# Kernel tuning notes

Hardware: AMD Instinct MI355X
Metric: run time of the kernel (lower is better)

The kernel has to match this reference:

```python
import jax, jax.numpy as jnp
import numpy as np

B, P, D, N, H = 1, 256, 512, 8, 64
STD = 0.02
IGNORE = -1000000.0


def setup_inputs() -> dict:
    key = jax.random.key(0)
    ks = jax.random.split(key, 9)
    inp = {"normalized_resid_pre": jax.random.normal(ks[0], (B, P, D), jnp.float32)}
    for i, s in enumerate("ABCDE"):
        inp["W_" + s] = STD * jax.random.normal(ks[i + 1], (N, D, H), jnp.float32)
        inp["b_" + s] = jnp.zeros((N, H), jnp.float32)
    inp["W_V"] = STD * jax.random.normal(ks[6], (N, H, H, H), jnp.float32)
    inp["W_K"] = STD * jax.random.normal(ks[7], (N, H, H, H), jnp.float32)
    inp["W_O"] = STD * jax.random.normal(ks[8], (N, H, D), jnp.float32)
    inp["b_O"] = jnp.zeros((D,), jnp.float32)
    return inp


def reference(normalized_resid_pre, W_A, b_A, W_B, b_B, W_C, b_C, W_D, b_D, W_E, b_E, W_V, W_K, W_O, b_O):
    x = normalized_resid_pre
    b_sz = x.shape[0]
    proj = lambda W, b: jnp.einsum('ndh,bpd->bpnh', W, x) + b
    ta = proj(W_A, b_A)
    tb = proj(W_B, b_B)
    tc = proj(W_C, b_C)
    td = proj(W_D, b_D)
    te = proj(W_E, b_E)
    # V_Layer: v[b, p1, p2, n, h3]
    v = jnp.einsum('bpnh,bqng,nhgf->bpqnf', td, te, W_V)
    # TrittentionCScore: chained einsums -> scores[b, n, p, q, r]
    step1 = jnp.einsum('brnk,nijk->brij', tc, W_K)
    step2 = jnp.einsum('brij,bqnj->briq', step1, tb)
    scores = jnp.einsum('briq,bpni->bnpqr', step2, ta)
    # CausalMask (attn_eq=False, order_attn=True): mask over (t=p, s=q, q=r) dims
    ti = jnp.arange(P)[:, None, None]
    si = jnp.arange(P)[None, :, None]
    qi = jnp.arange(P)[None, None, :]
    mask = (ti >= qi) | (si >= qi) | (ti >= si)  # [P, P, P]
    scores = jnp.where(mask, IGNORE, scores)
    # TrittentionCPattern: b n p q r -> b n r (p q), /d_head, extra column, softmax
    flat = jnp.transpose(scores, (0, 1, 4, 2, 3)).reshape(b_sz, N, P, P * P) / H
    extra = jnp.full((b_sz, N, P, 1), -1000.0, flat.dtype)
    attn = jax.nn.softmax(jnp.concatenate([flat, extra], axis=-1), axis=-1)
    # Z_Layer: v -> b n h (p s), extra zero column, combine
    vf = jnp.transpose(v, (0, 3, 4, 1, 2)).reshape(b_sz, N, H, P * P)
    vf = jnp.concatenate([vf, jnp.zeros((b_sz, N, H, 1), vf.dtype)], axis=-1)
    z = jnp.einsum('bnql,bnhl->bqnh', attn, vf)
    # Result + Out
    zint = jnp.einsum('bqnh,nhd->bqnd', z, W_O)
    return zint.sum(axis=2) + b_O
```

## Files before the change

### kernel.cpp

```cpp
#include <hip/hip_runtime.h>
#include <hip/hip_bf16.h>


typedef __hip_bfloat16 bf16;
typedef __attribute__((ext_vector_type(8))) short short8;
typedef __attribute__((ext_vector_type(4))) short s16x4;
typedef __attribute__((ext_vector_type(4))) float floatx4;

__device__ __forceinline__ float ldf(const float* p){ return *p; }
__device__ __forceinline__ float ldf(const bf16* p){ return __bfloat162float(*p); }
__device__ __forceinline__ void  stf(float* p, float v){ *p = v; }
__device__ __forceinline__ void  stf(bf16*  p, float v){ *p = __float2bfloat16(v); }

__device__ __forceinline__ floatx4 mfma16(short8 a, short8 b, floatx4 c){
  return __builtin_amdgcn_mfma_f32_16x16x32_bf16(a, b, c, 0, 0, 0);
}
__device__ __forceinline__ short8 ld_g8(const bf16* p){
  return *reinterpret_cast<const short8*>(p);
}
__device__ __forceinline__ short bfs(float x){
  bf16 v = __float2bfloat16(x);
  return *reinterpret_cast<short*>(&v);
}

__device__ __forceinline__ bool is_bf16_x(const void* xv)
{
  const unsigned* x32 = (const unsigned*)xv;
  unsigned w = x32[threadIdx.x & 63];
  unsigned lo = w & 0xFFFFu;
  unsigned e  = (lo >> 7) & 0xFFu;
  bool v = (lo == 0u) || (e >= 90u && e <= 145u);
  unsigned long long m = __ballot(v);
  return __popcll(m) >= 40;
}

template<typename TI>
__device__ __forceinline__ void proj_body(
    const TI* __restrict__ x, const TI* const* Ws, const TI* const* bs,
    bf16* __restrict__ tproj, float* As, float* Bs)
{
  const int bz = blockIdx.z, j = bz >> 3, n = bz & 7;
  const TI* B    = Ws[j] + (size_t)n * 32768;
  const TI* bias = bs[j] + n * 64;
  bf16* out = tproj + (size_t)j * 131072;
  const int m0 = blockIdx.y * 64;
  const int t = threadIdx.x, tx = t & 15, ty = t >> 4;
  float acc[4][4] = {};
  for (int k0 = 0; k0 < 512; k0 += 16) {
    { int m = t >> 2, kk = (t & 3) * 4;
      const TI* ap = x + (size_t)(m0 + m) * 512 + (k0 + kk);
      float a0 = ldf(ap+0), a1 = ldf(ap+1), a2 = ldf(ap+2), a3 = ldf(ap+3);
      As[(kk+0)*68+m] = a0; As[(kk+1)*68+m] = a1;
      As[(kk+2)*68+m] = a2; As[(kk+3)*68+m] = a3; }
    { int kk = t >> 4, nn = (t & 15) * 4;
      const TI* bp = B + (size_t)(k0 + kk) * 64 + nn;
      Bs[kk*68+nn+0] = ldf(bp+0); Bs[kk*68+nn+1] = ldf(bp+1);
      Bs[kk*68+nn+2] = ldf(bp+2); Bs[kk*68+nn+3] = ldf(bp+3); }
    __syncthreads();
    #pragma unroll
    for (int kk = 0; kk < 16; kk++) {
      float4 a4 = *reinterpret_cast<const float4*>(&As[kk*68 + ty*4]);
      float4 b4 = *reinterpret_cast<const float4*>(&Bs[kk*68 + tx*4]);
      float av[4] = {a4.x,a4.y,a4.z,a4.w}, bv[4] = {b4.x,b4.y,b4.z,b4.w};
      #pragma unroll
      for (int im = 0; im < 4; im++)
        #pragma unroll
        for (int in = 0; in < 4; in++) acc[im][in] += av[im] * bv[in];
    }
    __syncthreads();
  }
  #pragma unroll
  for (int im = 0; im < 4; im++)
    #pragma unroll
    for (int in = 0; in < 4; in++) {
      float v = acc[im][in] + ldf(bias + tx*4 + in);
      int p = m0 + ty*4 + im, h = tx*4 + in;
      if (j < 3) out[(size_t)p * 512 + n*64 + h] = __float2bfloat16(v);
      else       out[(size_t)n * 16384 + (size_t)h * 256 + p] = __float2bfloat16(v);
    }
}

__global__ __launch_bounds__(256) void proj_all(
    const void* __restrict__ x,
    const void* W0, const void* b0, const void* W1, const void* b1,
    const void* W2, const void* b2, const void* W3, const void* b3,
    const void* W4, const void* b4, bf16* __restrict__ tproj)
{
  __shared__ float As[16*68];
  __shared__ float Bs[16*68];
  if (is_bf16_x(x)) {
    const bf16* Ws[5] = {(const bf16*)W0,(const bf16*)W1,(const bf16*)W2,
                         (const bf16*)W3,(const bf16*)W4};
    const bf16* bs[5] = {(const bf16*)b0,(const bf16*)b1,(const bf16*)b2,
                         (const bf16*)b3,(const bf16*)b4};
    proj_body<bf16>((const bf16*)x, Ws, bs, tproj, As, Bs);
  } else {
    const float* Ws[5] = {(const float*)W0,(const float*)W1,(const float*)W2,
                          (const float*)W3,(const float*)W4};
    const float* bs[5] = {(const float*)b0,(const float*)b1,(const float*)b2,
                          (const float*)b3,(const float*)b4};
    proj_body<float>((const float*)x, Ws, bs, tproj, As, Bs);
  }
}

template<typename TW>
__device__ __forceinline__ void s1t_body(
    const bf16* __restrict__ tc, const TW* __restrict__ WK,
    bf16* __restrict__ s1t)
{
  const int i = blockIdx.x;
  const int t = threadIdx.x, wid = t >> 6, lane = t & 63, quad = lane >> 4, l16 = lane & 15;
  const int rw = blockIdx.y * 64 + wid * 16;
  floatx4 acc[4];
  #pragma unroll
  for (int jt = 0; jt < 4; jt++) acc[jt] = (floatx4){0.f, 0.f, 0.f, 0.f};
  for (int kc = 0; kc < 16; kc++) {
    short8 af = ld_g8(tc + (size_t)(rw + l16) * 512 + kc*32 + quad*8);
    const int n = kc >> 1, kk = (kc & 1) * 32 + quad * 8;
    #pragma unroll
    for (int jt = 0; jt < 4; jt++) {
      const TW* bp = WK + ((size_t)(n*64 + i) * 64 + jt*16 + l16) * 64 + kk;
      short8 bf;
      if constexpr (sizeof(TW) == 2) {
        bf = ld_g8((const bf16*)bp);
      } else {
        float4 x0 = *reinterpret_cast<const float4*>(bp);
        float4 x1 = *reinterpret_cast<const float4*>(bp + 4);
        bf[0]=bfs(x0.x); bf[1]=bfs(x0.y); bf[2]=bfs(x0.z); bf[3]=bfs(x0.w);
        bf[4]=bfs(x1.x); bf[5]=bfs(x1.y); bf[6]=bfs(x1.z); bf[7]=bfs(x1.w);
      }
      acc[jt] = mfma16(af, bf, acc[jt]);
    }
  }
  #pragma unroll
  for (int jt = 0; jt < 4; jt++)
    #pragma unroll
    for (int reg = 0; reg < 4; reg++)
      s1t[(size_t)(rw + quad*4 + reg) * 4096 + i*64 + jt*16 + l16] =
          __float2bfloat16(acc[jt][reg]);
}

__global__ __launch_bounds__(256) void s1t_all(
    const void* __restrict__ x, const bf16* __restrict__ tb,
    const bf16* __restrict__ tc, const void* __restrict__ WK,
    bf16* __restrict__ tbsbf, bf16* __restrict__ s1t)
{
  if (blockIdx.y == 4) {
    int t = blockIdx.x * 256 + threadIdx.x;
    int q = t >> 6, j = t & 63;
    float s = 0.f;
    #pragma unroll
    for (int n = 0; n < 8; n++) s += ldf(tb + q*512 + n*64 + j);
    tbsbf[t] = __float2bfloat16(s * 0.015625f);
    return;
  }
  if (is_bf16_x(x)) s1t_body<bf16>(tc, (const bf16*)WK, s1t);
  else              s1t_body<float>(tc, (const float*)WK, s1t);
}

__global__ __launch_bounds__(256) void tri_attn(
    const bf16* __restrict__ ta,
    const bf16* __restrict__ tbsbf,
    const bf16* __restrict__ s1t,
    const bf16* __restrict__ tdT,
    const bf16* __restrict__ teT,
    bf16* __restrict__ Sbuf)
{
  __shared__ __align__(16) char smb[39936];
  const int bx = blockIdx.x;
  const int n = bx & 7;
  const int r = 255 - (bx >> 3);
  const int t = threadIdx.x;
  const int wid = t >> 6, lane = t & 63, quad = lane >> 4, l16 = lane & 15;
  bf16* srow = Sbuf + (size_t)n * 1048576 + (size_t)r * 4096;
  if (r < 2) {
    short8 zz = (short8){0,0,0,0,0,0,0,0};
    reinterpret_cast<short8*>(srow)[t]       = zz;
    reinterpret_cast<short8*>(srow)[t + 256] = zz;
    return;
  }
  const int nch  = ((r - 1) >> 5) + 1;
  const int rcap = nch * 32;

  {
    const bf16* s1r = s1t + (size_t)r * 4096;
    short8 bfr[4][2];
    #pragma unroll
    for (int it = 0; it < 4; it++)
      #pragma unroll
      for (int kc = 0; kc < 2; kc++)
        bfr[it][kc] = ld_g8(s1r + (it*16 + l16)*64 + kc*32 + quad*8);
    #pragma unroll
    for (int qt = 0; qt < 4; qt++) {
      const int q0 = wid * 64 + qt * 16;
      if (q0 >= rcap) continue;
      if (q0 >= r) {
        #pragma unroll
        for (int it = 0; it < 4; it++)
          #pragma unroll
          for (int reg = 0; reg < 4; reg++) {
            int q = q0 + quad*4 + reg;
            *reinterpret_cast<bf16*>(smb + q*136 + (it*16 + l16)*2) =
                __float2bfloat16(0.f);
          }
        continue;
      }
      short8 af0 = ld_g8(tbsbf + (q0 + l16)*64 + quad*8);
      short8 af1 = ld_g8(tbsbf + (q0 + l16)*64 + 32 + quad*8);
      #pragma unroll
      for (int it = 0; it < 4; it++) {
        floatx4 acc = {0.f, 0.f, 0.f, 0.f};
        acc = mfma16(af0, bfr[it][0], acc);
        acc = mfma16(af1, bfr[it][1], acc);
        #pragma unroll
        for (int reg = 0; reg < 4; reg++) {
          int q = q0 + quad*4 + reg;
          float v = (q >= 1 && q < r) ? acc[reg] : 0.f;
          *reinterpret_cast<bf16*>(smb + q*136 + (it*16 + l16)*2) = __float2bfloat16(v);
        }
      }
    }
  }
  short8 taf[4][2];
  #pragma unroll
  for (int pt = 0; pt < 4; pt++)
    #pragma unroll
    for (int kc = 0; kc < 2; kc++)
      taf[pt][kc] = ld_g8(ta + (size_t)((pt*4 + wid)*16 + l16)*512 + n*64
                             + kc*32 + quad*8);
  __syncthreads();

  floatx4 Tacc[4][4];
  #pragma unroll
  for (int pt = 0; pt < 4; pt++)
    #pragma unroll
    for (int gt = 0; gt < 4; gt++) Tacc[pt][gt] = (floatx4){0.f, 0.f, 0.f, 0.f};
  float Zp = 0.f;
  char* EwB = smb + 34816 + wid * 1152;
  for (int ch = 0; ch < nch; ch++) {
    const int qc = ch * 32;
    if (qc + 31 <= wid * 16) continue;
    short8 cfr[2][2];
    #pragma unroll
    for (int qt2 = 0; qt2 < 2; qt2++)
      #pragma unroll
      for (int kc = 0; kc < 2; kc++)
        cfr[qt2][kc] = *reinterpret_cast<const short8*>(
            smb + (qc + qt2*16 + l16)*136 + (kc*32 + quad*8)*2);
    short8 tef[4];
    #pragma unroll
    for (int gt = 0; gt < 4; gt++)
      tef[gt] = ld_g8(teT + (size_t)n*16384 + (gt*16 + l16)*256 + qc + quad*8);
    #pragma unroll
    for (int pt = 0; pt < 4; pt++) {
      const int ptb = (pt*4 + wid) * 16;
      if (ptb >= qc + 31) continue;
      #pragma unroll
      for (int qt2 = 0; qt2 < 2; qt2++) {
        const int qh = qc + qt2*16;
        char* erow0 = EwB + (quad*4)*72 + (qt2*16 + l16)*2;
        if (qh + 15 <= ptb) {
          #pragma unroll
          for (int reg = 0; reg < 4; reg++)
            *reinterpret_cast<bf16*>(erow0 + reg*72) = __float2bfloat16(0.f);
        } else {
          floatx4 acc = {0.f, 0.f, 0.f, 0.f};
          acc = mfma16(taf[pt][0], cfr[qt2][0], acc);
          acc = mfma16(taf[pt][1], cfr[qt2][1], acc);
          if (qh >= ptb + 16 && qh + 15 < r) {
            #pragma unroll
            for (int reg = 0; reg < 4; reg++) {
              float e = __expf(acc[reg]);
              Zp += e;
              *reinterpret_cast<bf16*>(erow0 + reg*72) = __float2bfloat16(e);
            }
          } else {
            #pragma unroll
            for (int reg = 0; reg < 4; reg++) {
              int p = ptb + quad*4 + reg;
              int q = qh + l16;
              float e = (p < q && q < r) ? __expf(acc[reg]) : 0.f;
              Zp += e;
              *reinterpret_cast<bf16*>(erow0 + reg*72) = __float2bfloat16(e);
            }
          }
        }
      }
      short8 ef = *reinterpret_cast<const short8*>(EwB + l16*72 + quad*16);
      __builtin_amdgcn_s_setprio(1);
      #pragma unroll
      for (int gt = 0; gt < 4; gt++)
        Tacc[pt][gt] = mfma16(ef, tef[gt], Tacc[pt][gt]);
      __builtin_amdgcn_s_setprio(0);
    }
  }
  #pragma unroll
  for (int off = 32; off; off >>= 1) Zp += __shfl_down(Zp, off);
  float* scr = reinterpret_cast<float*>(smb + 39424);
  if (lane == 0) scr[wid] = Zp;
  __syncthreads();
  const float rinv = 1.f / (scr[0] + scr[1] + scr[2] + scr[3]);

  #pragma unroll
  for (int pt = 0; pt < 4; pt++) {
    if ((pt*4 + wid)*16 >= rcap) continue;
    #pragma unroll
    for (int gt = 0; gt < 4; gt++)
      #pragma unroll
      for (int reg = 0; reg < 4; reg++) {
        int g = gt*16 + l16;
        int p = (pt*4 + wid)*16 + quad*4 + reg;
        *reinterpret_cast<bf16*>(smb + g*528 + p*2) = __float2bfloat16(Tacc[pt][gt][reg]);
      }
  }
  __syncthreads();

  {
    short8 Taf[8];
    #pragma unroll
    for (int kc = 0; kc < 8; kc++)
      if (kc < nch)
        Taf[kc] = *reinterpret_cast<const short8*>(
            smb + (wid*16 + l16)*528 + (kc*32 + quad*8)*2);
    #pragma unroll
    for (int ht = 0; ht < 4; ht++) {
      floatx4 acc = {0.f, 0.f, 0.f, 0.f};
      __builtin_amdgcn_s_setprio(1);
      #pragma unroll
      for (int kc = 0; kc < 8; kc++) {
        if (kc < nch) {
          short8 bfragd = ld_g8(tdT + (size_t)n*16384 + (ht*16 + l16)*256 + kc*32 + quad*8);
          acc = mfma16(Taf[kc], bfragd, acc);
        }
      }
      __builtin_amdgcn_s_setprio(0);
      #pragma unroll
      for (int reg = 0; reg < 4; reg++) {
        int g = wid*16 + quad*4 + reg, h = ht*16 + l16;
        srow[h*64 + g] = __float2bfloat16(acc[reg] * rinv);
      }
    }
  }
}

template<typename TW>
__device__ __forceinline__ void z_body(
    const bf16* __restrict__ Sbuf, const TW* __restrict__ WV,
    float* __restrict__ zpart, int kslice, char* lds)
{
  const int rt = blockIdx.x, n = blockIdx.y, ks = blockIdx.z;
  const int t = threadIdx.x, wid = t >> 6, lane = t & 63, quad = lane >> 4, l16 = lane & 15;
  const int rw = rt * 64 + wid * 16;
  const int k0 = ks * kslice;
  const TW*  wvn = WV   + (size_t)n * 262144;
  const bf16* sn = Sbuf + (size_t)n * 1048576;
  floatx4 acc[4];
  #pragma unroll
  for (int ft = 0; ft < 4; ft++) acc[ft] = (floatx4){0.f, 0.f, 0.f, 0.f};
  const int row = t >> 3, f8 = (t & 7) * 8;
  for (int kb = k0; kb < k0 + kslice; kb += 32) {
    { const TW* src = wvn + (size_t)(kb + row) * 64 + f8;
      short sv[8];
      if constexpr (sizeof(TW) == 2) {
        short8 v = ld_g8((const bf16*)src);
        #pragma unroll
        for (int j = 0; j < 8; j++) sv[j] = v[j];
      } else {
        float4 a = *reinterpret_cast<const float4*>(src);
        float4 b = *reinterpret_cast<const float4*>(src + 4);
        sv[0]=bfs(a.x); sv[1]=bfs(a.y); sv[2]=bfs(a.z); sv[3]=bfs(a.w);
        sv[4]=bfs(b.x); sv[5]=bfs(b.y); sv[6]=bfs(b.z); sv[7]=bfs(b.w);
      }
      short* dst = reinterpret_cast<short*>(lds + row*136 + f8*2);
      s16x4 lo = {sv[0],sv[1],sv[2],sv[3]}, hi = {sv[4],sv[5],sv[6],sv[7]};
      *reinterpret_cast<s16x4*>(dst)     = lo;
      *reinterpret_cast<s16x4*>(dst + 4) = hi;
    }
    __syncthreads();
    short8 af = ld_g8(sn + (size_t)(rw + l16) * 4096 + kb + quad*8);
    #pragma unroll
    for (int ft = 0; ft < 4; ft++) {
      short8 bfv;
      #pragma unroll
      for (int j = 0; j < 8; j++)
        bfv[j] = *reinterpret_cast<const short*>(
            lds + (quad*8 + j)*136 + (ft*16 + l16)*2);
      acc[ft] = mfma16(af, bfv, acc[ft]);
    }
    __syncthreads();
  }
  float* zp = zpart + (size_t)ks * 131072;
  #pragma unroll
  for (int ft = 0; ft < 4; ft++)
    #pragma unroll
    for (int reg = 0; reg < 4; reg++)
      zp[(size_t)(rw + quad*4 + reg) * 512 + n*64 + ft*16 + l16] = acc[ft][reg];
}

__global__ __launch_bounds__(256) void z_all(
    const void* __restrict__ x, const bf16* __restrict__ Sbuf,
    const void* __restrict__ WV, float* __restrict__ zpart, int kslice)
{
  __shared__ __align__(16) char lds[32 * 136];
  if (is_bf16_x(x)) z_body<bf16>(Sbuf, (const bf16*)WV, zpart, kslice, lds);
  else              z_body<float>(Sbuf, (const float*)WV, zpart, kslice, lds);
}

__global__ __launch_bounds__(256) void zred_kern(
    const float* __restrict__ zpart, bf16* __restrict__ zbb, int ks)
{
  int idx = blockIdx.x * 256 + threadIdx.x;
  float s = 0.f;
  for (int k = 0; k < ks; k++) s += zpart[(size_t)k * 131072 + idx];
  zbb[idx] = __float2bfloat16(s);
}

template<typename TB, typename TC>
__device__ __forceinline__ void gemm_body(
    const bf16* __restrict__ A, const TB* __restrict__ B, TC* __restrict__ C,
    const TB* __restrict__ bias, float* As, float* Bs)
{
  const int m0 = blockIdx.y * 64, n0 = blockIdx.x * 64;
  const int t = threadIdx.x, tx = t & 15, ty = t >> 4;
  float acc[4][4] = {};
  for (int k0 = 0; k0 < 512; k0 += 16) {
    { int m = t >> 2, kk = (t & 3) * 4;
      const bf16* ap = A + (size_t)(m0 + m) * 512 + (k0 + kk);
      float a0 = ldf(ap+0), a1 = ldf(ap+1), a2 = ldf(ap+2), a3 = ldf(ap+3);
      As[(kk+0)*68+m] = a0; As[(kk+1)*68+m] = a1;
      As[(kk+2)*68+m] = a2; As[(kk+3)*68+m] = a3; }
    { int kk = t >> 4, nn = (t & 15) * 4;
      const TB* bp = B + (size_t)(k0 + kk) * 512 + (n0 + nn);
      Bs[kk*68+nn+0] = ldf(bp+0); Bs[kk*68+nn+1] = ldf(bp+1);
      Bs[kk*68+nn+2] = ldf(bp+2); Bs[kk*68+nn+3] = ldf(bp+3); }
    __syncthreads();
    #pragma unroll
    for (int kk = 0; kk < 16; kk++) {
      float4 a4 = *reinterpret_cast<const float4*>(&As[kk*68 + ty*4]);
      float4 b4 = *reinterpret_cast<const float4*>(&Bs[kk*68 + tx*4]);
      float av[4] = {a4.x,a4.y,a4.z,a4.w}, bv[4] = {b4.x,b4.y,b4.z,b4.w};
      #pragma unroll
      for (int im = 0; im < 4; im++)
        #pragma unroll
        for (int in = 0; in < 4; in++) acc[im][in] += av[im] * bv[in];
    }
    __syncthreads();
  }
  #pragma unroll
  for (int im = 0; im < 4; im++) {
    TC* cp = C + (size_t)(m0 + ty*4 + im) * 512 + n0 + tx*4;
    #pragma unroll
    for (int in = 0; in < 4; in++) {
      float v = acc[im][in] + ldf(bias + n0 + tx*4 + in);
      stf(cp + in, v);
    }
  }
}

__global__ __launch_bounds__(256) void gemm_all(
    const void* __restrict__ x, const bf16* __restrict__ zbb,
    const void* __restrict__ WO, const void* __restrict__ bO,
    void* __restrict__ out)
{
  __shared__ float As[16*68];
  __shared__ float Bs[16*68];
  if (is_bf16_x(x))
    gemm_body<bf16, bf16>(zbb, (const bf16*)WO, (bf16*)out, (const bf16*)bO, As, Bs);
  else
    gemm_body<float, float>(zbb, (const float*)WO, (float*)out, (const float*)bO, As, Bs);
}

extern "C" void kernel_launch(void* const* d_in, const int* in_sizes, int n_in,
                              void* d_out, int out_size, void* d_ws, size_t ws_size,
                              hipStream_t stream)
{
  (void)in_sizes; (void)n_in; (void)out_size;
  char* wsb = (char*)d_ws;
  bf16* tproj = (bf16*)(wsb + 256);
  bf16* tbsbf = (bf16*)(wsb + 1310976);
  bf16* s1t   = (bf16*)(wsb + 1343744);
  bf16* zbb   = (bf16*)(wsb + 3440896);
  bf16* Sbuf  = (bf16*)(wsb + 4194304);
  const long TE = 131072;
  const bool bigws = (ws_size == 0) || (ws_size >= 25165824);
  const int  ks     = bigws ? 8 : 2;
  const int  kslice = 4096 / ks;
  float* zpart = (float*)(bigws ? (wsb + 20971520) : (wsb + 1343744));

  proj_all<<<dim3(1,4,40), 256, 0, stream>>>(
      d_in[0], d_in[1], d_in[2], d_in[3], d_in[4], d_in[5], d_in[6],
      d_in[7], d_in[8], d_in[9], d_in[10], tproj);
  s1t_all<<<dim3(64,5), 256, 0, stream>>>(
      d_in[0], tproj + 1*TE, tproj + 2*TE, d_in[12], tbsbf, s1t);
  tri_attn<<<2048, 256, 0, stream>>>(
      tproj, tbsbf, s1t, tproj + 3*TE, tproj + 4*TE, Sbuf);
  z_all<<<dim3(4,8,ks), 256, 0, stream>>>(
      d_in[0], Sbuf, d_in[11], zpart, kslice);
  zred_kern<<<512, 256, 0, stream>>>(zpart, zbb, ks);
  gemm_all<<<dim3(8,4), 256, 0, stream>>>(
      d_in[0], zbb, d_in[13], d_in[14], d_out);
}
```

Before: 255.8 us.

## Pre-transpose W_V, add direct-MFMA z kernel, fuse split-K reduce into output GEMM

W_V is transposed to bf16 in an extra branch of the s1t kernel, so a new zmm kernel can compute z with direct global MFMA loads and two K-slices instead of the LDS-staged eight-slice path. The zred pass is dropped by having the output GEMM sum the two fp32 partials while loading A. In tri_attn, the softmax-exp tiles now go through two LDS buffers so two p-tiles' exp phases come before their MFMA updates, which should improve instruction overlap. This costs extra LDS per block and a W_V transpose on every call, and the old path stays as a fallback for small workspaces.

```diff
diff --git a/kernel.cpp b/kernel.cpp
--- a/kernel.cpp
+++ b/kernel.cpp
@@ -143,20 +143,82 @@
 __global__ __launch_bounds__(256) void s1t_all(
     const void* __restrict__ x, const bf16* __restrict__ tb,
     const bf16* __restrict__ tc, const void* __restrict__ WK,
-    bf16* __restrict__ tbsbf, bf16* __restrict__ s1t)
-{
+    bf16* __restrict__ tbsbf, bf16* __restrict__ s1t,
+    const void* __restrict__ WV, bf16* __restrict__ WVT)
+{
+  __shared__ short tile[64][72];
+  const int t = threadIdx.x;
   if (blockIdx.y == 4) {
-    int t = blockIdx.x * 256 + threadIdx.x;
-    int q = t >> 6, j = t & 63;
+    int tt = blockIdx.x * 256 + t;
+    int q = tt >> 6, j = tt & 63;
     float s = 0.f;
     #pragma unroll
     for (int n = 0; n < 8; n++) s += ldf(tb + q*512 + n*64 + j);
-    tbsbf[t] = __float2bfloat16(s * 0.015625f);
+    tbsbf[tt] = __float2bfloat16(s * 0.015625f);
+    return;
+  }
+  if (blockIdx.y == 5) {
+    const int n = blockIdx.x >> 3, kg = blockIdx.x & 7;
+    const bool bfp = is_bf16_x(x);
+    for (int sub = 0; sub < 8; sub++) {
+      const int k0 = kg*512 + sub*64;
+      { int kr = t >> 2, f16 = (t & 3) * 16;
+        if (bfp) {
+          const bf16* src = (const bf16*)WV + ((size_t)n*4096 + k0 + kr)*64 + f16;
+          *reinterpret_cast<short8*>(&tile[kr][f16])   = ld_g8(src);
+          *reinterpret_cast<short8*>(&tile[kr][f16+8]) = ld_g8(src + 8);
+        } else {
+          const float* src = (const float*)WV + ((size_t)n*4096 + k0 + kr)*64 + f16;
+          #pragma unroll
+          for (int j = 0; j < 16; j++) tile[kr][f16+j] = bfs(src[j]);
+        } }
+      __syncthreads();
+      { int f = t >> 2, k16 = (t & 3) * 16;
+        short8 w0, w1;
+        #pragma unroll
+        for (int j = 0; j < 8; j++) { w0[j] = tile[k16+j][f]; w1[j] = tile[k16+8+j][f]; }
+        bf16* dst = WVT + ((size_t)n*64 + f)*4096 + k0 + k16;
+        *reinterpret_cast<short8*>(dst)     = w0;
+        *reinterpret_cast<short8*>(dst + 8) = w1; }
+      __syncthreads();
+    }
     return;
   }
   if (is_bf16_x(x)) s1t_body<bf16>(tc, (const bf16*)WK, s1t);
   else              s1t_body<float>(tc, (const float*)WK, s1t);
 }
+
+#define E_PHASE(PT, BUF)                                                      \
+  {                                                                           \
+    const int ptb_ = ((PT)*4 + wid) * 16;                                     \
+    for (int qt2 = 0; qt2 < 2; qt2++) {                                       \
+      const int qh = qc + qt2*16;                                             \
+      char* erow0 = (BUF) + (quad*4)*72 + (qt2*16 + l16)*2;                   \
+      if (qh + 15 <= ptb_) {                                                  \
+        for (int reg = 0; reg < 4; reg++)                                     \
+          *reinterpret_cast<bf16*>(erow0 + reg*72) = __float2bfloat16(0.f);   \
+      } else {                                                                \
+        floatx4 acc = {0.f, 0.f, 0.f, 0.f};                                   \
+        acc = mfma16(taf[PT][0], cfr[qt2][0], acc);                           \
+        acc = mfma16(taf[PT][1], cfr[qt2][1], acc);                           \
+        if (qh >= ptb_ + 16 && qh + 15 < r) {                                 \
+          for (int reg = 0; reg < 4; reg++) {                                 \
+            float e = __expf(acc[reg]);                                       \
+            Zp += e;                                                          \
+            *reinterpret_cast<bf16*>(erow0 + reg*72) = __float2bfloat16(e);   \
+          }                                                                   \
+        } else {                                                              \
+          for (int reg = 0; reg < 4; reg++) {                                 \
+            int p = ptb_ + quad*4 + reg;                                      \
+            int q = qh + l16;                                                 \
+            float e = (p < q && q < r) ? __expf(acc[reg]) : 0.f;              \
+            Zp += e;                                                          \
+            *reinterpret_cast<bf16*>(erow0 + reg*72) = __float2bfloat16(e);   \
+          }                                                                   \
+        }                                                                     \
+      }                                                                       \
+    }                                                                         \
+  }
 
 __global__ __launch_bounds__(256) void tri_attn(
     const bf16* __restrict__ ta,
@@ -166,7 +228,7 @@
     const bf16* __restrict__ teT,
     bf16* __restrict__ Sbuf)
 {
-  __shared__ __align__(16) char smb[39936];
+  __shared__ __align__(16) char smb[44544];
   const int bx = blockIdx.x;
   const int n = bx & 7;
   const int r = 255 - (bx >> 3);
@@ -236,7 +298,8 @@
     #pragma unroll
     for (int gt = 0; gt < 4; gt++) Tacc[pt][gt] = (floatx4){0.f, 0.f, 0.f, 0.f};
   float Zp = 0.f;
-  char* EwB = smb + 34816 + wid * 1152;
+  char* bufA = smb + 34816 + wid * 2304;
+  char* bufB = bufA + 1152;
   for (int ch = 0; ch < nch; ch++) {
     const int qc = ch * 32;
     if (qc + 31 <= wid * 16) continue;
@@ -251,52 +314,45 @@
     #pragma unroll
     for (int gt = 0; gt < 4; gt++)
       tef[gt] = ld_g8(teT + (size_t)n*16384 + (gt*16 + l16)*256 + qc + quad*8);
-    #pragma unroll
-    for (int pt = 0; pt < 4; pt++) {
-      const int ptb = (pt*4 + wid) * 16;
-      if (ptb >= qc + 31) continue;
-      #pragma unroll
-      for (int qt2 = 0; qt2 < 2; qt2++) {
-        const int qh = qc + qt2*16;
-        char* erow0 = EwB + (quad*4)*72 + (qt2*16 + l16)*2;
-        if (qh + 15 <= ptb) {
-          #pragma unroll
-          for (int reg = 0; reg < 4; reg++)
-            *reinterpret_cast<bf16*>(erow0 + reg*72) = __float2bfloat16(0.f);
-        } else {
-          floatx4 acc = {0.f, 0.f, 0.f, 0.f};
-          acc = mfma16(taf[pt][0], cfr[qt2][0], acc);
-          acc = mfma16(taf[pt][1], cfr[qt2][1], acc);
-          if (qh >= ptb + 16 && qh + 15 < r) {
-            #pragma unroll
-            for (int reg = 0; reg < 4; reg++) {
-              float e = __expf(acc[reg]);
-              Zp += e;
-              *reinterpret_cast<bf16*>(erow0 + reg*72) = __float2bfloat16(e);
-            }
-          } else {
-            #pragma unroll
-            for (int reg = 0; reg < 4; reg++) {
-              int p = ptb + quad*4 + reg;
-              int q = qh + l16;
-              float e = (p < q && q < r) ? __expf(acc[reg]) : 0.f;
-              Zp += e;
-              *reinterpret_cast<bf16*>(erow0 + reg*72) = __float2bfloat16(e);
-            }
-          }
-        }
-      }
-      short8 ef = *reinterpret_cast<const short8*>(EwB + l16*72 + quad*16);
-      __builtin_amdgcn_s_setprio(1);
-      #pragma unroll
-      for (int gt = 0; gt < 4; gt++)
-        Tacc[pt][gt] = mfma16(ef, tef[gt], Tacc[pt][gt]);
-      __builtin_amdgcn_s_setprio(0);
+
+    {
+      const bool alive0 = ((0*4 + wid)*16 < qc + 31);
+      const bool alive1 = ((1*4 + wid)*16 < qc + 31);
+      short8 ef0, ef1;
+      if (alive0) { E_PHASE(0, bufA)
+                    ef0 = *reinterpret_cast<const short8*>(bufA + l16*72 + quad*16); }
+      if (alive1) { E_PHASE(1, bufB)
+                    ef1 = *reinterpret_cast<const short8*>(bufB + l16*72 + quad*16); }
+      if (alive0) { __builtin_amdgcn_s_setprio(1);
+        #pragma unroll
+        for (int gt = 0; gt < 4; gt++) Tacc[0][gt] = mfma16(ef0, tef[gt], Tacc[0][gt]);
+        __builtin_amdgcn_s_setprio(0); }
+      if (alive1) { __builtin_amdgcn_s_setprio(1);
+        #pragma unroll
+        for (int gt = 0; gt < 4; gt++) Tacc[1][gt] = mfma16(ef1, tef[gt], Tacc[1][gt]);
+        __builtin_amdgcn_s_setprio(0); }
+    }
+    {
+      const bool alive2 = ((2*4 + wid)*16 < qc + 31);
+      const bool alive3 = ((3*4 + wid)*16 < qc + 31);
+      short8 ef2, ef3;
+      if (alive2) { E_PHASE(2, bufA)
+                    ef2 = *reinterpret_cast<const short8*>(bufA + l16*72 + quad*16); }
+      if (alive3) { E_PHASE(3, bufB)
+                    ef3 = *reinterpret_cast<const short8*>(bufB + l16*72 + quad*16); }
+      if (alive2) { __builtin_amdgcn_s_setprio(1);
+        #pragma unroll
+        for (int gt = 0; gt < 4; gt++) Tacc[2][gt] = mfma16(ef2, tef[gt], Tacc[2][gt]);
+        __builtin_amdgcn_s_setprio(0); }
+      if (alive3) { __builtin_amdgcn_s_setprio(1);
+        #pragma unroll
+        for (int gt = 0; gt < 4; gt++) Tacc[3][gt] = mfma16(ef3, tef[gt], Tacc[3][gt]);
+        __builtin_amdgcn_s_setprio(0); }
     }
   }
   #pragma unroll
   for (int off = 32; off; off >>= 1) Zp += __shfl_down(Zp, off);
-  float* scr = reinterpret_cast<float*>(smb + 39424);
+  float* scr = reinterpret_cast<float*>(smb + 44032);
   if (lane == 0) scr[wid] = Zp;
   __syncthreads();
   const float rinv = 1.f / (scr[0] + scr[1] + scr[2] + scr[3]);
@@ -341,6 +397,29 @@
       }
     }
   }
+}
+
+__global__ __launch_bounds__(256) void zmm_kern(
+    const bf16* __restrict__ Sbuf, const bf16* __restrict__ WVT,
+    float* __restrict__ zpart)
+{
+  const int rt = blockIdx.x, n = blockIdx.y, ks = blockIdx.z;
+  const int t = threadIdx.x, wid = t >> 6, lane = t & 63, quad = lane >> 4, l16 = lane & 15;
+  const int rw = rt * 16;
+  const bf16* sn  = Sbuf + (size_t)n * 1048576;
+  const bf16* wvf = WVT + ((size_t)n*64 + wid*16 + l16) * 4096;
+  floatx4 acc = {0.f, 0.f, 0.f, 0.f};
+  const int k0 = ks * 2048;
+  #pragma unroll 4
+  for (int kb = k0; kb < k0 + 2048; kb += 32) {
+    short8 af = ld_g8(sn + (size_t)(rw + l16) * 4096 + kb + quad*8);
+    short8 bf = ld_g8(wvf + kb + quad*8);
+    acc = mfma16(af, bf, acc);
+  }
+  float* zp = zpart + (size_t)ks * 131072;
+  #pragma unroll
+  for (int reg = 0; reg < 4; reg++)
+    zp[(size_t)(rw + quad*4 + reg) * 512 + n*64 + wid*16 + l16] = acc[reg];
 }
 
 template<typename TW>
@@ -397,7 +476,7 @@
       zp[(size_t)(rw + quad*4 + reg) * 512 + n*64 + ft*16 + l16] = acc[ft][reg];
 }
 
-__global__ __launch_bounds__(256) void z_all(
+__global__ __launch_bounds__(256) void z_lds(
     const void* __restrict__ x, const bf16* __restrict__ Sbuf,
     const void* __restrict__ WV, float* __restrict__ zpart, int kslice)
 {
@@ -415,9 +494,9 @@
   zbb[idx] = __float2bfloat16(s);
 }
 
-template<typename TB, typename TC>
+template<int AMODE, typename TB, typename TC>
 __device__ __forceinline__ void gemm_body(
-    const bf16* __restrict__ A, const TB* __restrict__ B, TC* __restrict__ C,
+    const void* __restrict__ A, const TB* __restrict__ B, TC* __restrict__ C,
     const TB* __restrict__ bias, float* As, float* Bs)
 {
   const int m0 = blockIdx.y * 64, n0 = blockIdx.x * 64;
@@ -425,8 +504,17 @@
   float acc[4][4] = {};
   for (int k0 = 0; k0 < 512; k0 += 16) {
     { int m = t >> 2, kk = (t & 3) * 4;
-      const bf16* ap = A + (size_t)(m0 + m) * 512 + (k0 + kk);
-      float a0 = ldf(ap+0), a1 = ldf(ap+1), a2 = ldf(ap+2), a3 = ldf(ap+3);
+      size_t base = (size_t)(m0 + m) * 512 + (k0 + kk);
+      float a0, a1, a2, a3;
+      if constexpr (AMODE == 1) {
+        const float* zp = (const float*)A;
+        float4 u = *reinterpret_cast<const float4*>(zp + base);
+        float4 v = *reinterpret_cast<const float4*>(zp + 131072 + base);
+        a0 = u.x + v.x; a1 = u.y + v.y; a2 = u.z + v.z; a3 = u.w + v.w;
+      } else {
+        const bf16* zb = (const bf16*)A;
+        a0 = ldf(zb+base); a1 = ldf(zb+base+1); a2 = ldf(zb+base+2); a3 = ldf(zb+base+3);
+      }
       As[(kk+0)*68+m] = a0; As[(kk+1)*68+m] = a1;
       As[(kk+2)*68+m] = a2; As[(kk+3)*68+m] = a3; }
     { int kk = t >> 4, nn = (t & 15) * 4;
@@ -458,16 +546,23 @@
 }
 
 __global__ __launch_bounds__(256) void gemm_all(
-    const void* __restrict__ x, const bf16* __restrict__ zbb,
+    const void* __restrict__ x, const void* __restrict__ A,
     const void* __restrict__ WO, const void* __restrict__ bO,
-    void* __restrict__ out)
+    void* __restrict__ out, int amode)
 {
   __shared__ float As[16*68];
   __shared__ float Bs[16*68];
-  if (is_bf16_x(x))
-    gemm_body<bf16, bf16>(zbb, (const bf16*)WO, (bf16*)out, (const bf16*)bO, As, Bs);
-  else
-    gemm_body<float, float>(zbb, (const float*)WO, (float*)out, (const float*)bO, As, Bs);
+  if (is_bf16_x(x)) {
+    if (amode) gemm_body<1, bf16, bf16>(A, (const bf16*)WO, (bf16*)out,
+                                        (const bf16*)bO, As, Bs);
+    else       gemm_body<0, bf16, bf16>(A, (const bf16*)WO, (bf16*)out,
+                                        (const bf16*)bO, As, Bs);
+  } else {
+    if (amode) gemm_body<1, float, float>(A, (const float*)WO, (float*)out,
+                                          (const float*)bO, As, Bs);
+    else       gemm_body<0, float, float>(A, (const float*)WO, (float*)out,
+                                          (const float*)bO, As, Bs);
+  }
 }
 
 extern "C" void kernel_launch(void* const* d_in, const int* in_sizes, int n_in,
@@ -479,24 +574,30 @@
   bf16* tproj = (bf16*)(wsb + 256);
   bf16* tbsbf = (bf16*)(wsb + 1310976);
   bf16* s1t   = (bf16*)(wsb + 1343744);
+  float* zpart = (float*)(wsb + 1343744);
   bf16* zbb   = (bf16*)(wsb + 3440896);
   bf16* Sbuf  = (bf16*)(wsb + 4194304);
+  bf16* WVT   = (bf16*)(wsb + 20971520);
   const long TE = 131072;
   const bool bigws = (ws_size == 0) || (ws_size >= 25165824);
-  const int  ks     = bigws ? 8 : 2;
-  const int  kslice = 4096 / ks;
-  float* zpart = (float*)(bigws ? (wsb + 20971520) : (wsb + 1343744));
 
   proj_all<<<dim3(1,4,40), 256, 0, stream>>>(
       d_in[0], d_in[1], d_in[2], d_in[3], d_in[4], d_in[5], d_in[6],
       d_in[7], d_in[8], d_in[9], d_in[10], tproj);
-  s1t_all<<<dim3(64,5), 256, 0, stream>>>(
-      d_in[0], tproj + 1*TE, tproj + 2*TE, d_in[12], tbsbf, s1t);
+  s1t_all<<<dim3(64, bigws ? 6 : 5), 256, 0, stream>>>(
+      d_in[0], tproj + 1*TE, tproj + 2*TE, d_in[12], tbsbf, s1t,
+      d_in[11], WVT);
   tri_attn<<<2048, 256, 0, stream>>>(
       tproj, tbsbf, s1t, tproj + 3*TE, tproj + 4*TE, Sbuf);
-  z_all<<<dim3(4,8,ks), 256, 0, stream>>>(
-      d_in[0], Sbuf, d_in[11], zpart, kslice);
-  zred_kern<<<512, 256, 0, stream>>>(zpart, zbb, ks);
-  gemm_all<<<dim3(8,4), 256, 0, stream>>>(
-      d_in[0], zbb, d_in[13], d_in[14], d_out);
-}
+  if (bigws) {
+    zmm_kern<<<dim3(16,8,2), 256, 0, stream>>>(Sbuf, WVT, zpart);
+    gemm_all<<<dim3(8,4), 256, 0, stream>>>(
+        d_in[0], zpart, d_in[13], d_in[14], d_out, 1);
+  } else {
+    z_lds<<<dim3(4,8,2), 256, 0, stream>>>(
+        d_in[0], Sbuf, d_in[11], zpart, 2048);
+    zred_kern<<<512, 256, 0, stream>>>(zpart, zbb, 2);
+    gemm_all<<<dim3(8,4), 256, 0, stream>>>(
+        d_in[0], zbb, d_in[13], d_in[14], d_out, 0);
+  }
+}
```

After: 261.5 us. 2.2% more time.
